# Performance work log

Measured on AMD Instinct MI355X. Metric: run time of the kernel, lower is better.

Reference implementation:

```python
import jax, jax.numpy as jnp
import numpy as np

B, N, C, NUM_HEADS = 4, 2048, 768, 12
HID = 4 * C
EPS = 1e-5


def _ln(x, g, b):
    m = x.mean(-1, keepdims=True)
    v = ((x - m) ** 2).mean(-1, keepdims=True)
    return (x - m) / jnp.sqrt(v + EPS) * g + b


def _attend(q, k, v, scale):
    # q,k,v: (B, H, N, D)
    scores = jnp.einsum('bhnd,bhmd->bhnm', q, k) * scale
    a = jax.nn.softmax(scores, axis=-1)
    return jnp.einsum('bhnm,bhmd->bhnd', a, v)


def _split_heads(t):
    b, n, c = t.shape
    return t.reshape(b, n, NUM_HEADS, c // NUM_HEADS).transpose(0, 2, 1, 3)


def _merge_heads(t):
    b, h, n, d = t.shape
    return t.transpose(0, 2, 1, 3).reshape(b, n, h * d)


def setup_inputs() -> dict:
    key = jax.random.key(0)
    ks = jax.random.split(key, 16)
    s = 0.02
    inp = {
        'x': jax.random.normal(ks[0], (B, N, C), jnp.float32),
        'y': jax.random.normal(ks[1], (B, N, C), jnp.float32),
        'xpos': jax.random.randint(ks[2], (B, N, 2), 0, 64, jnp.int32),
        'ypos': jax.random.randint(ks[3], (B, N, 2), 0, 64, jnp.int32),
        'g1': jnp.ones((C,)), 'be1': jnp.zeros((C,)),
        'g2': jnp.ones((C,)), 'be2': jnp.zeros((C,)),
        'g3': jnp.ones((C,)), 'be3': jnp.zeros((C,)),
        'gy': jnp.ones((C,)), 'bey': jnp.zeros((C,)),
        'Wqkv': jax.random.normal(ks[4], (C, 3 * C), jnp.float32) * s,
        'Wo_sa': jax.random.normal(ks[5], (C, C), jnp.float32) * s,
        'bo_sa': jnp.zeros((C,)),
        'Wq': jax.random.normal(ks[6], (C, C), jnp.float32) * s,
        'Wk': jax.random.normal(ks[7], (C, C), jnp.float32) * s,
        'Wv': jax.random.normal(ks[8], (C, C), jnp.float32) * s,
        'Wo_ca': jax.random.normal(ks[9], (C, C), jnp.float32) * s,
        'bo_ca': jnp.zeros((C,)),
        'W1': jax.random.normal(ks[10], (C, HID), jnp.float32) * s,
        'b1': jnp.zeros((HID,)),
        'W2': jax.random.normal(ks[11], (HID, C), jnp.float32) * s,
        'b2': jnp.zeros((C,)),
        'h': 32, 'w': 64,
    }
    return inp


def reference(x, y, xpos, ypos, g1, be1, g2, be2, g3, be3, gy, bey,
              Wqkv, Wo_sa, bo_sa, Wq, Wk, Wv, Wo_ca, bo_ca,
              W1, b1, W2, b2, h, w):
    scale = (C // NUM_HEADS) ** -0.5
    # --- self attention (rope=None, dropout=0, drop_path=0) ---
    xn = _ln(x, g1, be1)
    qkv = (xn @ Wqkv).reshape(x.shape[0], x.shape[1], 3, C)
    q, k, v = (_split_heads(qkv[:, :, i]) for i in range(3))
    o = _merge_heads(_attend(q, k, v, scale)) @ Wo_sa + bo_sa
    x = x + o
    # --- cross attention ---
    yn = _ln(y, gy, bey)
    xn2 = _ln(x, g2, be2)
    qc = _split_heads(xn2 @ Wq)
    kc = _split_heads(yn @ Wk)
    vc = _split_heads(yn @ Wv)
    oc = _merge_heads(_attend(qc, kc, vc, scale)) @ Wo_ca + bo_ca
    x = x + oc
    # --- MLP (exact GELU as torch nn.GELU default) ---
    xn3 = _ln(x, g3, be3)
    x = x + (jax.nn.gelu(xn3 @ W1 + b1, approximate=False) @ W2 + b2)
    return x
```

## Files before the change

### kernel.cpp

```cpp
#include <hip/hip_runtime.h>
#include <math.h>

typedef unsigned short u16;
typedef __attribute__((ext_vector_type(4))) float f32x4;
typedef __attribute__((ext_vector_type(8))) __bf16 bf16x8;
typedef __attribute__((ext_vector_type(8))) short s16x8;

#define AS1 __attribute__((address_space(1)))
#define AS3 __attribute__((address_space(3)))

__device__ __forceinline__ u16 cvt(float f) {
  __bf16 h = (__bf16)f;
  return *(u16*)&h;
}

__device__ __forceinline__ unsigned cvtpk(float lo, float hi) {
  unsigned r;
  asm("v_cvt_pk_bf16_f32 %0, %1, %2" : "=v"(r) : "v"(lo), "v"(hi));
  return r;
}

__device__ __forceinline__ float fexp2(float x) {
  float r;
  asm volatile("v_exp_f32 %0, %1" : "=v"(r) : "v"(x));
  return r;
}

__device__ __forceinline__ void load_lds16(const void* g, void* l) {
  __builtin_amdgcn_global_load_lds((AS1 void*)g, (AS3 void*)l, 16, 0, 0);
}

__device__ __forceinline__ f32x4 mfma16(bf16x8 a, bf16x8 b, f32x4 c) {
  return __builtin_amdgcn_mfma_f32_16x16x32_bf16(a, b, c, 0, 0, 0);
}

struct WT8 {
  const float* src[8];
  u16* dst[8];
  int K[8];
  int N[8];
  int cnt[8];
};

__global__ void wtrans_all(WT8 a) {
  __shared__ float t[32][33];
  int rem = blockIdx.x, i = 0;
  while (rem >= a.cnt[i]) { rem -= a.cnt[i]; ++i; }
  const int nb = a.N[i] >> 5;
  const int n0 = (rem % nb) * 32, k0 = (rem / nb) * 32;
  const float* W = a.src[i];
  u16* WT = a.dst[i];
  const int K = a.K[i], N = a.N[i];
  for (int r = threadIdx.y; r < 32; r += 8)
    t[r][threadIdx.x] = W[(size_t)(k0 + r) * N + n0 + threadIdx.x];
  __syncthreads();
  for (int r = threadIdx.y; r < 32; r += 8)
    WT[(size_t)(n0 + r) * K + k0 + threadIdx.x] = cvt(t[threadIdx.x][r]);
}

__global__ __launch_bounds__(256)
void ln_bf16(const float* __restrict__ in, const float* __restrict__ g,
             const float* __restrict__ be, u16* __restrict__ out) {
  const int row = blockIdx.x, tid = threadIdx.x;
  const float* x = in + (size_t)row * 768;
  float v0 = x[tid], v1 = x[tid + 256], v2 = x[tid + 512];
  float s = v0 + v1 + v2;
  for (int m = 1; m < 64; m <<= 1) s += __shfl_xor(s, m);
  __shared__ float red[8];
  const int w = tid >> 6, lane = tid & 63;
  if (lane == 0) red[w] = s;
  __syncthreads();
  s = red[0] + red[1] + red[2] + red[3];
  const float mean = s * (1.f / 768.f);
  const float d0 = v0 - mean, d1 = v1 - mean, d2 = v2 - mean;
  float q = d0 * d0 + d1 * d1 + d2 * d2;
  for (int m = 1; m < 64; m <<= 1) q += __shfl_xor(q, m);
  if (lane == 0) red[4 + w] = q;
  __syncthreads();
  q = red[4] + red[5] + red[6] + red[7];
  const float rstd = rsqrtf(q * (1.f / 768.f) + 1e-5f);
  u16* o = out + (size_t)row * 768;
  o[tid]       = cvt(d0 * rstd * g[tid]       + be[tid]);
  o[tid + 256] = cvt(d1 * rstd * g[tid + 256] + be[tid + 256]);
  o[tid + 512] = cvt(d2 * rstd * g[tid + 512] + be[tid + 512]);
}

template <int EPI, int BM>
__global__ __launch_bounds__(256, BM == 128 ? 2 : 3)
void gemm_bt(const u16* __restrict__ A, const u16* __restrict__ BT,
             const float* __restrict__ bias, const float* resid,
             void* outp, int M, int N, int K, int ldc) {
  constexpr int NI = (BM == 128) ? 4 : 2;
  __shared__ u16 As[BM * 32];
  __shared__ u16 Bs[128 * 32];
  const int tid = threadIdx.x;
  const int lane = tid & 63, w = tid >> 6;
  const int row0 = blockIdx.y * BM, col0 = blockIdx.x * 128;
  const int wm = (BM == 128) ? (w >> 1) * 64 : 0;
  const int wn = (BM == 128) ? (w & 1) * 64 : w * 32;
  const int lr = lane & 15, lk = (lane >> 4) * 8;
  const int srow = lane >> 2, scol = (lane & 3) * 8;

  f32x4 acc[4][NI] = {};

  for (int k0 = 0; k0 < K; k0 += 32) {
    if (BM == 128) {
#pragma unroll
      for (int i = 0; i < 2; ++i) {
        const int chunk = w * 2 + i;
        load_lds16(A + (size_t)(row0 + chunk * 16 + srow) * K + k0 + scol, &As[chunk * 512]);
        load_lds16(BT + (size_t)(col0 + chunk * 16 + srow) * K + k0 + scol, &Bs[chunk * 512]);
      }
    } else {
      load_lds16(A + (size_t)(row0 + w * 16 + srow) * K + k0 + scol, &As[w * 512]);
#pragma unroll
      for (int i = 0; i < 2; ++i) {
        const int chunk = w * 2 + i;
        load_lds16(BT + (size_t)(col0 + chunk * 16 + srow) * K + k0 + scol, &Bs[chunk * 512]);
      }
    }
    __syncthreads();
    bf16x8 af[4], bf[NI];
#pragma unroll
    for (int mi = 0; mi < 4; ++mi) af[mi] = *(const bf16x8*)&As[(wm + mi * 16 + lr) * 32 + lk];
#pragma unroll
    for (int ni = 0; ni < NI; ++ni) bf[ni] = *(const bf16x8*)&Bs[(wn + ni * 16 + lr) * 32 + lk];
#pragma unroll
    for (int mi = 0; mi < 4; ++mi)
#pragma unroll
      for (int ni = 0; ni < NI; ++ni)
        acc[mi][ni] = mfma16(af[mi], bf[ni], acc[mi][ni]);
    __syncthreads();
  }

  const int rbase = (lane >> 4) * 4;
#pragma unroll
  for (int mi = 0; mi < 4; ++mi) {
#pragma unroll
    for (int ni = 0; ni < NI; ++ni) {
#pragma unroll
      for (int rr = 0; rr < 4; ++rr) {
        const int r = row0 + wm + mi * 16 + rbase + rr;
        const int c = col0 + wn + ni * 16 + lr;
        float v = acc[mi][ni][rr];
        if (EPI == 0) {
          ((u16*)outp)[(size_t)r * ldc + c] = cvt(v);
        } else if (EPI == 1) {
          ((float*)outp)[(size_t)r * ldc + c] = v + bias[c] + resid[(size_t)r * ldc + c];
        } else {
          v += bias[c];
          v = 0.5f * v * (1.f + erff(v * 0.70710678118654752f));
          ((u16*)outp)[(size_t)r * ldc + c] = cvt(v);
        }
      }
    }
  }
}

__global__ __launch_bounds__(256, 3)
void flash_attn(const u16* __restrict__ qk, const u16* __restrict__ vt, u16* __restrict__ out) {
  __shared__ u16 Ks[2][64 * 64];
  __shared__ u16 Vs[2][64 * 64];
  __shared__ u16 P[128 * 72];
  const int tid = threadIdx.x, lane = tid & 63, w = tid >> 6;
  const int b = blockIdx.z, h = blockIdx.y, qb = blockIdx.x;
  const u16* qp = qk + (size_t)b * 2048 * 1536 + h * 64;
  const u16* kp = qp + 768;
  const u16* vtp = vt + (size_t)(h * 64) * 8192 + b * 2048;
  const int lr = lane & 15, g = lane >> 4, lk = g * 8;
  const int qrow = qb * 128 + w * 32;

  bf16x8 qf[2][2];
#pragma unroll
  for (int gq = 0; gq < 2; ++gq) {
#pragma unroll
    for (int t = 0; t < 2; ++t) {
      s16x8 qr = *(const s16x8*)&qp[(size_t)(qrow + gq * 16 + lr) * 1536 + t * 32 + lk];
      bf16x8 f;
#pragma unroll
      for (int j = 0; j < 8; ++j) {
        unsigned u = (unsigned)(u16)qr[j] << 16;
        f[j] = (__bf16)(__uint_as_float(u) * 0.18033688f);
      }
      qf[gq][t] = f;
    }
  }

  bf16x8 onesf;
#pragma unroll
  for (int j = 0; j < 8; ++j) onesf[j] = (__bf16)1.0f;

  f32x4 o[2][4] = {};
  f32x4 o4[2] = {};
  float rowm[2] = {-1e30f, -1e30f};

#define STAGE(bi, kv)                                                          \
  do {                                                                         \
    _Pragma("unroll") for (int i_ = 0; i_ < 2; ++i_) {                         \
      const int ch = i_ * 256 + tid;                                           \
      const int r_ = ch >> 3, c_ = ch & 7, cs_ = c_ ^ (r_ & 7);                \
      load_lds16(kp + (size_t)((kv) + r_) * 1536 + cs_ * 8, &Ks[bi][ch * 8]);  \
      load_lds16(vtp + (size_t)r_ * 8192 + (kv) + cs_ * 8, &Vs[bi][ch * 8]);   \
    }                                                                          \
  } while (0)

  STAGE(0, 0);
  __syncthreads();
  int cur = 0;

  for (int kv0 = 0; kv0 < 2048; kv0 += 64) {
    if (kv0 + 64 < 2048) STAGE(cur ^ 1, kv0 + 64);

    f32x4 s[2][4] = {};
#pragma unroll
    for (int t = 0; t < 2; ++t) {
#pragma unroll
      for (int ni = 0; ni < 4; ++ni) {
        const int r = ni * 16 + lr;
        bf16x8 kf = *(const bf16x8*)&Ks[cur][r * 64 + ((4 * t + g) ^ (lr & 7)) * 8];
        s[0][ni] = mfma16(kf, qf[0][t], s[0][ni]);
        s[1][ni] = mfma16(kf, qf[1][t], s[1][ni]);
      }
    }

    float lm[2];
#pragma unroll
    for (int gq = 0; gq < 2; ++gq) {
      float m0 = fmaxf(fmaxf(s[gq][0][0], s[gq][0][1]), fmaxf(s[gq][0][2], s[gq][0][3]));
      float m1 = fmaxf(fmaxf(s[gq][1][0], s[gq][1][1]), fmaxf(s[gq][1][2], s[gq][1][3]));
      float m2 = fmaxf(fmaxf(s[gq][2][0], s[gq][2][1]), fmaxf(s[gq][2][2], s[gq][2][3]));
      float m3 = fmaxf(fmaxf(s[gq][3][0], s[gq][3][1]), fmaxf(s[gq][3][2], s[gq][3][3]));
      lm[gq] = fmaxf(fmaxf(m0, m1), fmaxf(m2, m3));
    }
    const int ok = (lm[0] <= rowm[0] + 8.f) & (lm[1] <= rowm[1] + 8.f);
    if (!__all(ok)) {
#pragma unroll
      for (int gq = 0; gq < 2; ++gq) {
        float v = lm[gq];
        v = fmaxf(v, __shfl_xor(v, 16));
        v = fmaxf(v, __shfl_xor(v, 32));
        const float mn = fmaxf(rowm[gq], v);
        const float alpha = fexp2(rowm[gq] - mn);
        rowm[gq] = mn;
#pragma unroll
        for (int di = 0; di < 4; ++di) o[gq][di] *= alpha;
        o4[gq] *= alpha;
      }
    }

    unsigned* Pw = (unsigned*)P;
#pragma unroll
    for (int gq = 0; gq < 2; ++gq) {
      const int qrl = w * 32 + gq * 16 + lr;
#pragma unroll
      for (int ni = 0; ni < 4; ++ni) {
#pragma unroll
        for (int r = 0; r < 2; ++r) {
          const float p0 = fexp2(s[gq][ni][2 * r] - rowm[gq]);
          const float p1 = fexp2(s[gq][ni][2 * r + 1] - rowm[gq]);
          Pw[(qrl * 72 + ni * 16 + 4 * g + 2 * r) >> 1] = cvtpk(p0, p1);
        }
      }
    }

#pragma unroll
    for (int t = 0; t < 2; ++t) {
      bf16x8 pb0 = *(const bf16x8*)&P[(w * 32 + lr) * 72 + t * 32 + g * 8];
      bf16x8 pb1 = *(const bf16x8*)&P[(w * 32 + 16 + lr) * 72 + t * 32 + g * 8];
#pragma unroll
      for (int di = 0; di < 4; ++di) {
        bf16x8 va = *(const bf16x8*)&Vs[cur][(di * 16 + lr) * 64 + ((4 * t + g) ^ (lr & 7)) * 8];
        o[0][di] = mfma16(va, pb0, o[0][di]);
        o[1][di] = mfma16(va, pb1, o[1][di]);
      }
      o4[0] = mfma16(onesf, pb0, o4[0]);
      o4[1] = mfma16(onesf, pb1, o4[1]);
    }

    __syncthreads();
    cur ^= 1;
  }
#undef STAGE

#pragma unroll
  for (int gq = 0; gq < 2; ++gq) {
    const float inv = 1.0f / o4[gq][0];
    const size_t n = (size_t)b * 2048 + qrow + gq * 16 + lr;
#pragma unroll
    for (int di = 0; di < 4; ++di) {
      uint2 uv;
      uv.x = cvtpk(o[gq][di][0] * inv, o[gq][di][1] * inv);
      uv.y = cvtpk(o[gq][di][2] * inv, o[gq][di][3] * inv);
      *(uint2*)&out[n * 768 + h * 64 + di * 16 + 4 * g] = uv;
    }
  }
}

extern "C" void kernel_launch(void* const* d_in, const int* in_sizes, int n_in,
                              void* d_out, int out_size, void* d_ws, size_t ws_size,
                              hipStream_t stream) {
  const float* x     = (const float*)d_in[0];
  const float* y     = (const float*)d_in[1];
  const float* g1    = (const float*)d_in[4];
  const float* be1   = (const float*)d_in[5];
  const float* g2    = (const float*)d_in[6];
  const float* be2   = (const float*)d_in[7];
  const float* g3    = (const float*)d_in[8];
  const float* be3   = (const float*)d_in[9];
  const float* gy    = (const float*)d_in[10];
  const float* bey   = (const float*)d_in[11];
  const float* Wqkv  = (const float*)d_in[12];
  const float* Wo_sa = (const float*)d_in[13];
  const float* bo_sa = (const float*)d_in[14];
  const float* Wq    = (const float*)d_in[15];
  const float* Wk    = (const float*)d_in[16];
  const float* Wv    = (const float*)d_in[17];
  const float* Wo_ca = (const float*)d_in[18];
  const float* bo_ca = (const float*)d_in[19];
  const float* W1    = (const float*)d_in[20];
  const float* b1    = (const float*)d_in[21];
  const float* W2    = (const float*)d_in[22];
  const float* b2    = (const float*)d_in[23];

  u16* WqkvT = (u16*)d_ws;
  u16* WoSaT = WqkvT + (size_t)2304 * 768;
  u16* WqT   = WoSaT + (size_t)768 * 768;
  u16* WkT   = WqT   + (size_t)768 * 768;
  u16* WvT   = WkT   + (size_t)768 * 768;
  u16* WoCaT = WvT   + (size_t)768 * 768;
  u16* W1T   = WoCaT + (size_t)768 * 768;
  u16* W2T   = W1T   + (size_t)3072 * 768;
  u16* R1    = W2T   + (size_t)768 * 3072;
  u16* VT    = R1    + (size_t)8192 * 1536;
  u16* R2    = R1    + (size_t)8192 * 3072;
  u16* R3    = R2    + (size_t)8192 * 768;
  float* xo  = (float*)d_out;

  WT8 wa;
  {
    const float* s8[8] = {Wqkv, Wo_sa, Wq, Wk, Wv, Wo_ca, W1, W2};
    u16* d8[8] = {WqkvT, WoSaT, WqT, WkT, WvT, WoCaT, W1T, W2T};
    const int K8[8] = {768, 768, 768, 768, 768, 768, 768, 3072};
    const int N8[8] = {2304, 768, 768, 768, 768, 768, 3072, 768};
    for (int i = 0; i < 8; ++i) {
      wa.src[i] = s8[i]; wa.dst[i] = d8[i];
      wa.K[i] = K8[i]; wa.N[i] = N8[i];
      wa.cnt[i] = (N8[i] / 32) * (K8[i] / 32);
    }
  }
  wtrans_all<<<9216, dim3(32, 8), 0, stream>>>(wa);

  ln_bf16<<<8192, 256, 0, stream>>>(x, g1, be1, R2);
  gemm_bt<0, 128><<<dim3(12, 64), 256, 0, stream>>>(R2, WqkvT, nullptr, nullptr, R1, 8192, 1536, 768, 1536);
  gemm_bt<0, 64><<<dim3(64, 12), 256, 0, stream>>>(WqkvT + (size_t)1536 * 768, R2, nullptr, nullptr, VT, 768, 8192, 768, 8192);
  flash_attn<<<dim3(16, 12, 4), 256, 0, stream>>>(R1, VT, R2);
  gemm_bt<1, 64><<<dim3(6, 128), 256, 0, stream>>>(R2, WoSaT, bo_sa, x, xo, 8192, 768, 768, 768);

  ln_bf16<<<8192, 256, 0, stream>>>(y, gy, bey, R3);
  ln_bf16<<<8192, 256, 0, stream>>>(xo, g2, be2, R2);
  gemm_bt<0, 64><<<dim3(6, 128), 256, 0, stream>>>(R2, WqT, nullptr, nullptr, R1, 8192, 768, 768, 1536);
  gemm_bt<0, 64><<<dim3(6, 128), 256, 0, stream>>>(R3, WkT, nullptr, nullptr, R1 + 768, 8192, 768, 768, 1536);
  gemm_bt<0, 64><<<dim3(64, 12), 256, 0, stream>>>(WvT, R3, nullptr, nullptr, VT, 768, 8192, 768, 8192);
  flash_attn<<<dim3(16, 12, 4), 256, 0, stream>>>(R1, VT, R3);
  gemm_bt<1, 64><<<dim3(6, 128), 256, 0, stream>>>(R3, WoCaT, bo_ca, xo, xo, 8192, 768, 768, 768);

  ln_bf16<<<8192, 256, 0, stream>>>(xo, g3, be3, R2);
  gemm_bt<2, 128><<<dim3(24, 64), 256, 0, stream>>>(R2, W1T, b1, nullptr, R1, 8192, 3072, 768, 3072);
  gemm_bt<1, 64><<<dim3(6, 128), 256, 0, stream>>>(R1, W2T, b2, xo, xo, 8192, 768, 3072, 768);
}
```

Before: 515.7 us.

## Deepen BM=64 GEMM K-tile to 64 with XOR-swizzled LDS and block remap

For the BM=64 GEMM variant, the K step per iteration grows from 32 to 64. This halves the barrier count and loop overhead per unit of work. LDS rows are XOR-swizzled on store and load so that the wider 128-byte rows do not cause bank conflicts on the MFMA fragment reads. Workgroup IDs are also remapped in groups of 8 to change how tiles are assigned across the XCDs. The trade-off is double the LDS per block, which may reduce occupancy.

Result: faster. 467.9 us (-9.3%).

```diff
diff --git a/kernel.cpp b/kernel.cpp
--- a/kernel.cpp
+++ b/kernel.cpp
@@ -91,49 +91,91 @@
              const float* __restrict__ bias, const float* resid,
              void* outp, int M, int N, int K, int ldc) {
   constexpr int NI = (BM == 128) ? 4 : 2;
-  __shared__ u16 As[BM * 32];
-  __shared__ u16 Bs[128 * 32];
+  constexpr int BK = (BM == 128) ? 32 : 64;
+  __shared__ u16 As[BM * BK];
+  __shared__ u16 Bs[128 * BK];
   const int tid = threadIdx.x;
   const int lane = tid & 63, w = tid >> 6;
-  const int row0 = blockIdx.y * BM, col0 = blockIdx.x * 128;
+  const int lr = lane & 15, g = lane >> 4;
+
+  int bx = blockIdx.x, by = blockIdx.y;
+  if (BM == 64) {
+    const int nwg = gridDim.x * gridDim.y;
+    if ((nwg & 7) == 0) {
+      const int d = by * gridDim.x + bx;
+      const int l = (d & 7) * (nwg >> 3) + (d >> 3);
+      bx = l % gridDim.x;
+      by = l / gridDim.x;
+    }
+  }
+  const int row0 = by * BM, col0 = bx * 128;
   const int wm = (BM == 128) ? (w >> 1) * 64 : 0;
   const int wn = (BM == 128) ? (w & 1) * 64 : w * 32;
-  const int lr = lane & 15, lk = (lane >> 4) * 8;
-  const int srow = lane >> 2, scol = (lane & 3) * 8;
 
   f32x4 acc[4][NI] = {};
 
-  for (int k0 = 0; k0 < K; k0 += 32) {
-    if (BM == 128) {
+  if (BM == 128) {
+    const int srow = lane >> 2, scol = (lane & 3) * 8;
+    const int lk = g * 8;
+    for (int k0 = 0; k0 < K; k0 += 32) {
 #pragma unroll
       for (int i = 0; i < 2; ++i) {
         const int chunk = w * 2 + i;
         load_lds16(A + (size_t)(row0 + chunk * 16 + srow) * K + k0 + scol, &As[chunk * 512]);
         load_lds16(BT + (size_t)(col0 + chunk * 16 + srow) * K + k0 + scol, &Bs[chunk * 512]);
       }
-    } else {
-      load_lds16(A + (size_t)(row0 + w * 16 + srow) * K + k0 + scol, &As[w * 512]);
+      __syncthreads();
+      bf16x8 af[4], bf[NI];
+#pragma unroll
+      for (int mi = 0; mi < 4; ++mi) af[mi] = *(const bf16x8*)&As[(wm + mi * 16 + lr) * 32 + lk];
+#pragma unroll
+      for (int ni = 0; ni < NI; ++ni) bf[ni] = *(const bf16x8*)&Bs[(wn + ni * 16 + lr) * 32 + lk];
+#pragma unroll
+      for (int mi = 0; mi < 4; ++mi)
+#pragma unroll
+        for (int ni = 0; ni < NI; ++ni)
+          acc[mi][ni] = mfma16(af[mi], bf[ni], acc[mi][ni]);
+      __syncthreads();
+    }
+  } else {
+    for (int k0 = 0; k0 < K; k0 += 64) {
 #pragma unroll
       for (int i = 0; i < 2; ++i) {
-        const int chunk = w * 2 + i;
-        load_lds16(BT + (size_t)(col0 + chunk * 16 + srow) * K + k0 + scol, &Bs[chunk * 512]);
-      }
-    }
-    __syncthreads();
-    bf16x8 af[4], bf[NI];
-#pragma unroll
-    for (int mi = 0; mi < 4; ++mi) af[mi] = *(const bf16x8*)&As[(wm + mi * 16 + lr) * 32 + lk];
-#pragma unroll
-    for (int ni = 0; ni < NI; ++ni) bf[ni] = *(const bf16x8*)&Bs[(wn + ni * 16 + lr) * 32 + lk];
-#pragma unroll
-    for (int mi = 0; mi < 4; ++mi)
-#pragma unroll
-      for (int ni = 0; ni < NI; ++ni)
-        acc[mi][ni] = mfma16(af[mi], bf[ni], acc[mi][ni]);
-    __syncthreads();
-  }
-
-  const int rbase = (lane >> 4) * 4;
+        const int ch = i * 256 + tid;
+        const int r = ch >> 3, c = ch & 7, cs = c ^ (r & 7);
+        load_lds16(A + (size_t)(row0 + r) * K + k0 + cs * 8, &As[ch * 8]);
+      }
+#pragma unroll
+      for (int i = 0; i < 4; ++i) {
+        const int ch = i * 256 + tid;
+        const int r = ch >> 3, c = ch & 7, cs = c ^ (r & 7);
+        load_lds16(BT + (size_t)(col0 + r) * K + k0 + cs * 8, &Bs[ch * 8]);
+      }
+      __syncthreads();
+#pragma unroll
+      for (int kk = 0; kk < 2; ++kk) {
+        bf16x8 af[4], bf[NI];
+#pragma unroll
+        for (int mi = 0; mi < 4; ++mi) {
+          const int r = mi * 16 + lr;
+          af[mi] = *(const bf16x8*)&As[r * 64 + (((kk * 4 + g) ^ (r & 7)) * 8)];
+        }
+#pragma unroll
+        for (int ni = 0; ni < NI; ++ni) {
+          const int r = wn + ni * 16 + lr;
+          bf[ni] = *(const bf16x8*)&Bs[r * 64 + (((kk * 4 + g) ^ (r & 7)) * 8)];
+        }
+#pragma unroll
+        for (int mi = 0; mi < 4; ++mi)
+#pragma unroll
+          for (int ni = 0; ni < NI; ++ni)
+            acc[mi][ni] = mfma16(af[mi], bf[ni], acc[mi][ni]);
+      }
+      __syncthreads();
+    }
+  }
+
+  const int rbase = g * 4;
 #pragma unroll
   for (int mi = 0; mi < 4; ++mi) {
 #pragma unroll
```
